# Performance work log

Hardware: AMD Instinct MI355X
Metric: run time of the kernel (lower is better)

The kernel has to match this reference:

```python
import jax, jax.numpy as jnp
import numpy as np

B, T, L, D = 2, 16, 256, 1152
NH, HD = 16, 72
MLP_H = int(int(D * 4.0) * 2 / 3)  # 3072, per SwiGLUFFN


def _rms(x, w, eps=1e-6):
    return x * jax.lax.rsqrt(jnp.mean(jnp.square(x), axis=-1, keepdims=True) + eps) * w


def _attn(x, qkv_w, qkv_b, qn, kn, proj_w, proj_b, nh):
    Bn, N, C = x.shape
    hd = C // nh
    qkv = (x @ qkv_w + qkv_b).reshape(Bn, N, 3, nh, hd)
    qkv = jnp.transpose(qkv, (2, 0, 3, 1, 4))  # [3, Bn, nh, N, hd]
    q, k, v = qkv[0], qkv[1], qkv[2]
    q = _rms(q, qn)
    k = _rms(k, kn)
    scores = jnp.einsum('bhnd,bhmd->bhnm', q, k) / jnp.sqrt(jnp.float32(hd))
    a = jax.nn.softmax(scores, axis=-1)
    o = jnp.einsum('bhnm,bhmd->bhnd', a, v)
    o = jnp.transpose(o, (0, 2, 1, 3)).reshape(Bn, N, C)
    return o @ proj_w + proj_b


def setup_inputs() -> dict:
    key = jax.random.key(0)
    ks = jax.random.split(key, 12)
    w = lambda k, shape: jax.random.normal(k, shape, jnp.float32) * 0.02
    return {
        'x': jax.random.normal(ks[0], (B, T, L, D), jnp.float32),
        'c': jax.random.normal(ks[1], (B, D), jnp.float32),
        'norm1_w': jnp.ones((D,), jnp.float32),
        'norm2_w': jnp.ones((D,), jnp.float32),
        'norm3_w': jnp.ones((D,), jnp.float32),
        'qn_s': jnp.ones((HD,), jnp.float32),
        'kn_s': jnp.ones((HD,), jnp.float32),
        'qkv_s_w': w(ks[2], (D, 3 * D)),
        'qkv_s_b': jnp.zeros((3 * D,), jnp.float32),
        'proj_s_w': w(ks[3], (D, D)),
        'proj_s_b': jnp.zeros((D,), jnp.float32),
        'qn_t': jnp.ones((HD,), jnp.float32),
        'kn_t': jnp.ones((HD,), jnp.float32),
        'qkv_t_w': w(ks[4], (D, 3 * D)),
        'qkv_t_b': jnp.zeros((3 * D,), jnp.float32),
        'proj_t_w': w(ks[5], (D, D)),
        'proj_t_b': jnp.zeros((D,), jnp.float32),
        'w12_w': w(ks[6], (D, 2 * MLP_H)),
        'w12_b': jnp.zeros((2 * MLP_H,), jnp.float32),
        'w3_w': w(ks[7], (MLP_H, D)),
        'w3_b': jnp.zeros((D,), jnp.float32),
        'ada_w': w(ks[8], (D, 9 * D)),
        'ada_b': jnp.zeros((9 * D,), jnp.float32),
    }


def reference(x, c, norm1_w, norm2_w, norm3_w,
              qn_s, kn_s, qkv_s_w, qkv_s_b, proj_s_w, proj_s_b,
              qn_t, kn_t, qkv_t_w, qkv_t_b, proj_t_w, proj_t_b,
              w12_w, w12_b, w3_w, w3_b, ada_w, ada_b):
    Bb, Tt, Ll, Dd = x.shape
    # adaLN_modulation: SiLU then Linear, chunk into 9 [B, D] tensors
    ch = (jax.nn.silu(c) @ ada_w + ada_b).reshape(Bb, 9, Dd)
    sh_s, sc_s, g_s = ch[:, 0], ch[:, 1], ch[:, 2]
    sh_t, sc_t, g_t = ch[:, 3], ch[:, 4], ch[:, 5]
    sh_m, sc_m, g_m = ch[:, 6], ch[:, 7], ch[:, 8]

    # spatial attention over L, folded batch B*T
    x_s = x.reshape(Bb * Tt, Ll, Dd)
    shs = jnp.repeat(sh_s, Tt, axis=0)[:, None, :]   # [B*T,1,D]
    scs = jnp.repeat(sc_s, Tt, axis=0)[:, None, :]
    gs = jnp.repeat(g_s, Tt, axis=0)[:, None, :]
    xn = _rms(x_s, norm1_w) * (1 + scs) + shs
    x_s = x_s + gs * _attn(xn, qkv_s_w, qkv_s_b, qn_s, kn_s, proj_s_w, proj_s_b, NH)
    x = x_s.reshape(Bb, Tt, Ll, Dd)

    # temporal attention over T, folded batch B*L
    x_t = jnp.transpose(x, (0, 2, 1, 3)).reshape(Bb * Ll, Tt, Dd)
    sht = jnp.repeat(sh_t, Ll, axis=0)[:, None, :]
    sct = jnp.repeat(sc_t, Ll, axis=0)[:, None, :]
    gt = jnp.repeat(g_t, Ll, axis=0)[:, None, :]
    xn = _rms(x_t, norm2_w) * (1 + sct) + sht
    x_t = x_t + gt * _attn(xn, qkv_t_w, qkv_t_b, qn_t, kn_t, proj_t_w, proj_t_b, NH)
    x = jnp.transpose(x_t.reshape(Bb, Ll, Tt, Dd), (0, 2, 1, 3))

    # SwiGLU MLP with adaLN modulate + gate
    xn = _rms(x, norm3_w) * (1 + sc_m[:, None, None, :]) + sh_m[:, None, None, :]
    x12 = xn @ w12_w + w12_b
    x1, x2 = jnp.split(x12, 2, axis=-1)
    mlp_out = (jax.nn.silu(x1) * x2) @ w3_w + w3_b
    x = x + g_m[:, None, None, :] * mlp_out
    return x
```

## Files before the change

kernel.cpp:

```cpp
#include <hip/hip_runtime.h>
#include <stdint.h>

typedef __bf16 bf16x8 __attribute__((ext_vector_type(8)));
typedef float f32x4 __attribute__((ext_vector_type(4)));

__device__ __forceinline__ float b2f(uint32_t u) {
  union { uint32_t i; float f; } v; v.i = u << 16; return v.f;
}
__device__ __forceinline__ uint16_t f2b(float f) {
  union { float f; uint32_t i; } v; v.f = f;
  uint32_t r = (v.i + 0x7fffu + ((v.i >> 16) & 1u)) >> 16;
  return (uint16_t)r;
}
__device__ __forceinline__ void unpack8(uint4 u, float* f) {
  f[0] = b2f(u.x & 0xffffu); f[1] = b2f(u.x >> 16);
  f[2] = b2f(u.y & 0xffffu); f[3] = b2f(u.y >> 16);
  f[4] = b2f(u.z & 0xffffu); f[5] = b2f(u.z >> 16);
  f[6] = b2f(u.w & 0xffffu); f[7] = b2f(u.w >> 16);
}

__device__ __forceinline__ void gl2lds16(const void* g, void* l) {
  __builtin_amdgcn_global_load_lds(
      (const __attribute__((address_space(1))) void*)g,
      (__attribute__((address_space(3))) void*)l, 16, 0, 0);
}

__global__ __launch_bounds__(512, 2) void gemm256_k(
    const uint16_t* __restrict__ A, int lda,
    const uint16_t* __restrict__ Bt,
    const float* __restrict__ bias,
    uint16_t* __restrict__ outb,
    float* __restrict__ outf, const float* __restrict__ resid,
    const float* __restrict__ gate,
    int N, int K, int mode)
{
  __shared__ __align__(16) uint16_t L[65536];
  const int tid = threadIdx.x;
  const int lane = tid & 63, wave = tid >> 6;
  const int l15 = lane & 15, quad = lane >> 4;
  const int wm = (wave >> 2) * 128, wn = (wave & 3) * 64;

  const int xcd = blockIdx.x & 7;
  const int slot = blockIdx.x >> 3;
  const int mt = xcd * 4 + (slot & 3);
  const int nt = slot >> 2;
  const int row0 = mt * 256, col0 = nt * 256;

  const int NTk = K >> 6;

  const uint16_t* Ag = A + (size_t)row0 * lda;
  const uint16_t* Bg = Bt + (size_t)col0 * K;

  const int sX = (lane & 7) ^ (lane >> 3);
  const int laneRowA = lane >> 3;
  const int laneK8A = sX * 8;
  const int laneRowB = 2 * (lane >> 3) + ((sX >> 2) & 1);
  const int laneK8B = (sX & 3) * 8;
  const int rA0 = ((wave * 16) & 63) + (((wave * 16) >> 6) << 7);
  const int rB0 = wave * 32;

#define STAGE_A(BUF, SUB, KT) do { \
    const uint16_t* g_ = Ag + (size_t)(rA0 + (SUB) * 64 + laneRowA) * lda + (size_t)(KT) * 64 + laneK8A; \
    uint16_t* l_ = (uint16_t*)&L[(BUF) * 32768 + (rA0 + (SUB) * 64) * 64]; \
    gl2lds16(g_, l_); \
    gl2lds16(g_ + (size_t)8 * lda, l_ + 512); \
  } while (0)

#define STAGE_B(BUF, HALF, KT) do { \
    const uint16_t* g_ = Bg + (size_t)(rB0 + laneRowB) * K + (size_t)(KT) * 64 + (HALF) * 32 + laneK8B; \
    uint16_t* l_ = (uint16_t*)&L[(BUF) * 32768 + 16384 + (HALF) * 8192 + rB0 * 32]; \
    gl2lds16(g_, l_); \
    gl2lds16(g_ + (size_t)16 * K, l_ + 512); \
  } while (0)

  f32x4 acc[8][4];
#pragma unroll
  for (int i = 0; i < 8; i++)
#pragma unroll
    for (int j = 0; j < 4; j++)
      acc[i][j] = (f32x4){0.f, 0.f, 0.f, 0.f};

  bf16x8 a_[4], b_[4];

#define PHASE(CUR, KK, QM, READB, STAGE_STMT, VM_STMT) do { \
    _Pragma("unroll") for (int mi = 0; mi < 4; mi++) \
      a_[mi] = *(const bf16x8*)&L[(CUR) * 32768 + (wm + (QM) * 64 + mi * 16 + l15) * 64 + \
                                  ((((KK) * 4 + quad) ^ (l15 & 7)) * 8)]; \
    if (READB) { \
      _Pragma("unroll") for (int ni = 0; ni < 4; ni++) \
        b_[ni] = *(const bf16x8*)&L[(CUR) * 32768 + 16384 + (KK) * 8192 + \
                                    ((wn >> 1) + ni * 8 + (l15 >> 1)) * 64 + \
                                    ((((((l15 & 1) << 2) | quad)) ^ (l15 >> 1)) * 8)]; \
    } \
    STAGE_STMT; \
    __builtin_amdgcn_sched_barrier(0); \
    __builtin_amdgcn_s_barrier(); \
    asm volatile("s_waitcnt lgkmcnt(0)" ::: "memory"); \
    __builtin_amdgcn_sched_barrier(0); \
    __builtin_amdgcn_s_setprio(1); \
    _Pragma("unroll") for (int mi = 0; mi < 4; mi++) \
      _Pragma("unroll") for (int ni = 0; ni < 4; ni++) \
        acc[(QM) * 4 + mi][ni] = __builtin_amdgcn_mfma_f32_16x16x32_bf16( \
            a_[mi], b_[ni], acc[(QM) * 4 + mi][ni], 0, 0, 0); \
    __builtin_amdgcn_s_setprio(0); \
    __builtin_amdgcn_sched_barrier(0); \
    VM_STMT; \
    __builtin_amdgcn_sched_barrier(0); \
    __builtin_amdgcn_s_barrier(); \
    __builtin_amdgcn_sched_barrier(0); \
  } while (0)

#define TILE(CUR, T) do { \
    PHASE(CUR, 0, 0, 1, { if ((T) + 1 < NTk) STAGE_B((CUR) ^ 1, 1, (T) + 1); }, {}); \
    PHASE(CUR, 0, 1, 0, { if ((T) + 1 < NTk) STAGE_A((CUR) ^ 1, 1, (T) + 1); }, {}); \
    PHASE(CUR, 1, 0, 1, { if ((T) + 2 < NTk) STAGE_B((CUR), 0, (T) + 2); }, {}); \
    PHASE(CUR, 1, 1, 0, { if ((T) + 2 < NTk) STAGE_A((CUR), 0, (T) + 2); }, \
      { if ((T) + 2 < NTk) { asm volatile("s_waitcnt vmcnt(4)" ::: "memory"); } \
        else               { asm volatile("s_waitcnt vmcnt(0)" ::: "memory"); } }); \
  } while (0)

  STAGE_A(0, 0, 0); STAGE_A(0, 1, 0); STAGE_B(0, 0, 0); STAGE_B(0, 1, 0);
  STAGE_A(1, 0, 1); STAGE_B(1, 0, 1);
  asm volatile("s_waitcnt vmcnt(4)" ::: "memory");
  __builtin_amdgcn_sched_barrier(0);
  __builtin_amdgcn_s_barrier();
  __builtin_amdgcn_sched_barrier(0);

  for (int t = 0; t < NTk; t += 2) {
    TILE(0, t);
    TILE(1, t + 1);
  }

#undef PHASE
#undef TILE
#undef STAGE_A
#undef STAGE_B

#pragma unroll
  for (int mi = 0; mi < 8; mi++) {
#pragma unroll
    for (int ni = 0; ni < 4; ni++) {
      const int colg = col0 + wn + ni * 16 + l15;
      if (colg < N) {
        const float bv = bias ? bias[colg] : 0.f;
#pragma unroll
        for (int i = 0; i < 4; i++) {
          const int rowg = row0 + wm + mi * 16 + quad * 4 + i;
          const float v = acc[mi][ni][i] + bv;
          const size_t idx = (size_t)rowg * N + colg;
          if (mode == 0) {
            outb[idx] = f2b(v);
          } else {
            const int b = rowg >> 12;
            outf[idx] = resid[idx] + gate[b * 10368 + colg] * v;
          }
        }
      }
    }
  }
}

__global__ __launch_bounds__(256) void rmsnorm_k(
    const float* __restrict__ x, const float* __restrict__ w,
    const float* __restrict__ chv, int shsel, int scsel,
    uint16_t* __restrict__ xn)
{
  const int row = blockIdx.x;
  const int b = row >> 12;
  const float* xr = x + (size_t)row * 1152;
  float ss = 0.f;
  for (int d = threadIdx.x; d < 1152; d += 256) { const float v = xr[d]; ss += v * v; }
  for (int off = 32; off > 0; off >>= 1) ss += __shfl_down(ss, off);
  __shared__ float red[4];
  if ((threadIdx.x & 63) == 0) red[threadIdx.x >> 6] = ss;
  __syncthreads();
  const float tot = red[0] + red[1] + red[2] + red[3];
  const float rs = rsqrtf(tot * (1.f / 1152.f) + 1e-6f);
  const float* sh = chv + b * 10368 + shsel * 1152;
  const float* sc = chv + b * 10368 + scsel * 1152;
  uint16_t* xo = xn + (size_t)row * 1152;
  for (int d = threadIdx.x; d < 1152; d += 256)
    xo[d] = f2b(xr[d] * rs * w[d] * (1.f + sc[d]) + sh[d]);
}

__global__ __launch_bounds__(256) void qknorm_k(
    uint16_t* __restrict__ qkv, const float* __restrict__ qn, const float* __restrict__ kn)
{
  const int tid = threadIdx.x;
  const int rl = tid >> 5, unit = tid & 31;
  const int h = unit & 15, isK = unit >> 4;
  const size_t row = (size_t)blockIdx.x * 8 + rl;
  uint16_t* p = qkv + row * 3456 + isK * 1152 + h * 72;
  const float* w = isK ? kn : qn;
  float v[72];
#pragma unroll
  for (int i = 0; i < 9; i++) unpack8(((const uint4*)p)[i], v + i * 8);
  float ss = 0.f;
#pragma unroll
  for (int d = 0; d < 72; d++) ss += v[d] * v[d];
  const float rs = rsqrtf(ss * (1.f / 72.f) + 1e-6f);
#pragma unroll
  for (int d = 0; d < 72; d++) p[d] = f2b(v[d] * rs * w[d]);
}

#define AK_STRIDE 104
#define VT_STRIDE 88
#define PS_STRIDE 72
__global__ __launch_bounds__(256) void attn_s_k(
    const uint16_t* __restrict__ qkv, uint16_t* __restrict__ out)
{
  __shared__ __align__(16) uint16_t Ks[64 * AK_STRIDE];
  __shared__ __align__(16) uint16_t Vt[80 * VT_STRIDE];
  __shared__ __align__(16) uint16_t Ps[4 * 64 * PS_STRIDE];
  const int bh = blockIdx.x;
  const int bt = bh >> 4, h = bh & 15;
  const int tid = threadIdx.x;
  const int lane = tid & 63, wave = tid >> 6;
  const int l15 = lane & 15, quad = lane >> 4;
  const size_t rowbase = (size_t)bt * 256;
  const float scale = 0.1178511301977579f;

  union { uint4 u; bf16x8 v; } zu; zu.u = make_uint4(0, 0, 0, 0);
  const bf16x8 zero8 = zu.v;

  bf16x8 qf[4][3];
#pragma unroll
  for (int mi = 0; mi < 4; mi++) {
    const uint16_t* qp = qkv + (rowbase + wave * 64 + mi * 16 + l15) * 3456 + h * 72;
    qf[mi][0] = *(const bf16x8*)(qp + quad * 8);
    qf[mi][1] = *(const bf16x8*)(qp + 32 + quad * 8);
    qf[mi][2] = (quad == 0) ? *(const bf16x8*)(qp + 64) : zero8;
  }

  f32x4 oacc[4][5];
#pragma unroll
  for (int mi = 0; mi < 4; mi++)
#pragma unroll
    for (int dt = 0; dt < 5; dt++)
      oacc[mi][dt] = (f32x4){0.f, 0.f, 0.f, 0.f};
  float mrun[4][4], lrun[4][4];
#pragma unroll
  for (int mi = 0; mi < 4; mi++)
#pragma unroll
    for (int i = 0; i < 4; i++) { mrun[mi][i] = -1e30f; lrun[mi][i] = 0.f; }

  uint16_t* psw = &Ps[wave * 64 * PS_STRIDE];

  for (int c = 0; c < 4; c++) {
    __syncthreads();
    for (int idx = tid; idx < 576; idx += 256) {
      const int rr = idx / 9, cc = idx - rr * 9;
      const uint16_t* kg = qkv + (rowbase + c * 64 + rr) * 3456 + 1152 + h * 72 + cc * 8;
      *(uint4*)&Ks[rr * AK_STRIDE + cc * 8] = *(const uint4*)kg;
      uint4 vv = *(const uint4*)(kg + 1152);
      const uint16_t* e = (const uint16_t*)&vv;
#pragma unroll
      for (int j = 0; j < 8; j++) Vt[(cc * 8 + j) * VT_STRIDE + rr] = e[j];
    }
    __syncthreads();

    f32x4 s[4][4];
#pragma unroll
    for (int mi = 0; mi < 4; mi++)
#pragma unroll
      for (int ni = 0; ni < 4; ni++)
        s[mi][ni] = (f32x4){0.f, 0.f, 0.f, 0.f};
#pragma unroll
    for (int ni = 0; ni < 4; ni++) {
      bf16x8 kf0 = *(const bf16x8*)&Ks[(ni * 16 + l15) * AK_STRIDE + quad * 8];
      bf16x8 kf1 = *(const bf16x8*)&Ks[(ni * 16 + l15) * AK_STRIDE + 32 + quad * 8];
      bf16x8 kf2 = (quad == 0) ? *(const bf16x8*)&Ks[(ni * 16 + l15) * AK_STRIDE + 64] : zero8;
#pragma unroll
      for (int mi = 0; mi < 4; mi++) {
        s[mi][ni] = __builtin_amdgcn_mfma_f32_16x16x32_bf16(qf[mi][0], kf0, s[mi][ni], 0, 0, 0);
        s[mi][ni] = __builtin_amdgcn_mfma_f32_16x16x32_bf16(qf[mi][1], kf1, s[mi][ni], 0, 0, 0);
        s[mi][ni] = __builtin_amdgcn_mfma_f32_16x16x32_bf16(qf[mi][2], kf2, s[mi][ni], 0, 0, 0);
      }
    }

#pragma unroll
    for (int mi = 0; mi < 4; mi++) {
#pragma unroll
      for (int i = 0; i < 4; i++) {
        float mx = fmaxf(fmaxf(s[mi][0][i], s[mi][1][i]), fmaxf(s[mi][2][i], s[mi][3][i])) * scale;
#pragma unroll
        for (int d = 1; d < 16; d <<= 1) mx = fmaxf(mx, __shfl_xor(mx, d));
        const float mnew = fmaxf(mrun[mi][i], mx);
        const float corr = __expf(mrun[mi][i] - mnew);
        mrun[mi][i] = mnew;
        float psum = 0.f;
#pragma unroll
        for (int ni = 0; ni < 4; ni++) {
          const float p = __expf(s[mi][ni][i] * scale - mnew);
          s[mi][ni][i] = p;
          psum += p;
        }
#pragma unroll
        for (int d = 1; d < 16; d <<= 1) psum += __shfl_xor(psum, d);
        lrun[mi][i] = lrun[mi][i] * corr + psum;
#pragma unroll
        for (int dt = 0; dt < 5; dt++) oacc[mi][dt][i] *= corr;
      }
    }

#pragma unroll
    for (int mi = 0; mi < 4; mi++)
#pragma unroll
      for (int ni = 0; ni < 4; ni++)
#pragma unroll
        for (int i = 0; i < 4; i++)
          psw[(mi * 16 + quad * 4 + i) * PS_STRIDE + ni * 16 + l15] = f2b(s[mi][ni][i]);

#pragma unroll
    for (int kk = 0; kk < 2; kk++) {
      bf16x8 pf[4];
#pragma unroll
      for (int mi = 0; mi < 4; mi++)
        pf[mi] = *(const bf16x8*)&psw[(mi * 16 + l15) * PS_STRIDE + kk * 32 + quad * 8];
#pragma unroll
      for (int dt = 0; dt < 5; dt++) {
        bf16x8 vf = *(const bf16x8*)&Vt[(dt * 16 + l15) * VT_STRIDE + kk * 32 + quad * 8];
#pragma unroll
        for (int mi = 0; mi < 4; mi++)
          oacc[mi][dt] = __builtin_amdgcn_mfma_f32_16x16x32_bf16(pf[mi], vf, oacc[mi][dt], 0, 0, 0);
      }
    }
  }

#pragma unroll
  for (int mi = 0; mi < 4; mi++) {
#pragma unroll
    for (int i = 0; i < 4; i++) {
      const float inv = 1.f / lrun[mi][i];
      const size_t orow = rowbase + wave * 64 + mi * 16 + quad * 4 + i;
#pragma unroll
      for (int dt = 0; dt < 5; dt++) {
        const int d = dt * 16 + l15;
        if (d < 72) out[orow * 1152 + h * 72 + d] = f2b(oacc[mi][dt][i] * inv);
      }
    }
  }
}

__global__ __launch_bounds__(128) void attn_t_k(
    const uint16_t* __restrict__ qkv, uint16_t* __restrict__ out)
{
  const int blk = blockIdx.x;
  const int bl = blk >> 1, hg = blk & 1;
  const int b = bl >> 8, l = bl & 255;
  const int tid = threadIdx.x;
  const int hh = tid >> 4, tq = tid & 15;
  const int h = hg * 8 + hh;
  __shared__ __align__(16) uint16_t kb[8 * 16 * 72];
  __shared__ __align__(16) uint16_t vb[8 * 16 * 72];

#pragma unroll
  for (int it = 0; it < 9; it++) {
    const int idx = tid + it * 128;
    const int rowL = idx / 9, cc = idx % 9;
    const int hhL = rowL >> 4, tL = rowL & 15;
    const size_t grow = (size_t)b * 4096 + (size_t)tL * 256 + l;
    const int colk = 1152 + (hg * 8 + hhL) * 72 + cc * 8;
    ((uint4*)&kb[rowL * 72])[cc] = *(const uint4*)(qkv + grow * 3456 + colk);
    ((uint4*)&vb[rowL * 72])[cc] = *(const uint4*)(qkv + grow * 3456 + colk + 1152);
  }
  __syncthreads();

  float q[72];
  const size_t qrow = (size_t)b * 4096 + (size_t)tq * 256 + l;
  {
    const uint16_t* qp = qkv + qrow * 3456 + h * 72;
#pragma unroll
    for (int i = 0; i < 9; i++) unpack8(((const uint4*)qp)[i], q + i * 8);
  }
  const float scale = 0.1178511301977579f;
  float s[16];
#pragma unroll
  for (int m = 0; m < 16; m++) {
    const uint4* kr = (const uint4*)&kb[(hh * 16 + m) * 72];
    float a = 0.f;
#pragma unroll
    for (int i = 0; i < 9; i++) {
      float kf[8]; unpack8(kr[i], kf);
#pragma unroll
      for (int j = 0; j < 8; j++) a += q[i * 8 + j] * kf[j];
    }
    s[m] = a * scale;
  }
  float mx = -1e30f;
#pragma unroll
  for (int m = 0; m < 16; m++) mx = fmaxf(mx, s[m]);
  float sum = 0.f;
#pragma unroll
  for (int m = 0; m < 16; m++) { s[m] = __expf(s[m] - mx); sum += s[m]; }
  const float inv = 1.f / sum;
  float o[72];
#pragma unroll
  for (int d = 0; d < 72; d++) o[d] = 0.f;
#pragma unroll
  for (int m = 0; m < 16; m++) {
    const float p = s[m];
    const uint4* vr = (const uint4*)&vb[(hh * 16 + m) * 72];
#pragma unroll
    for (int i = 0; i < 9; i++) {
      float vf[8]; unpack8(vr[i], vf);
#pragma unroll
      for (int j = 0; j < 8; j++) o[i * 8 + j] += p * vf[j];
    }
  }
  uint16_t* op = out + qrow * 1152 + h * 72;
#pragma unroll
  for (int d = 0; d < 72; d++) op[d] = f2b(o[d] * inv);
}

__global__ __launch_bounds__(256) void transcvt_k(
    const float* __restrict__ in, uint16_t* __restrict__ out, int K, int N)
{
  __shared__ float t[32][33];
  const int n0 = blockIdx.x * 32, k0 = blockIdx.y * 32;
  const int tx = threadIdx.x & 31, ty = threadIdx.x >> 5;
#pragma unroll
  for (int i = 0; i < 32; i += 8)
    t[ty + i][tx] = in[(size_t)(k0 + ty + i) * N + n0 + tx];
  __syncthreads();
#pragma unroll
  for (int i = 0; i < 32; i += 8)
    out[(size_t)(n0 + ty + i) * K + k0 + tx] = f2b(t[tx][ty + i]);
}

__global__ __launch_bounds__(256) void swiglu_k(uint16_t* __restrict__ x12)
{
  const size_t gid = (size_t)blockIdx.x * 256 + threadIdx.x;
  const size_t row = gid / 384, c8 = gid - row * 384;
  uint4* base = (uint4*)(x12 + row * 6144);
  float a[8], bb[8];
  unpack8(base[c8], a);
  unpack8(base[384 + c8], bb);
  uint32_t r[4];
#pragma unroll
  for (int j = 0; j < 4; j++) {
    const float s0 = a[2 * j]     / (1.f + __expf(-a[2 * j]))     * bb[2 * j];
    const float s1 = a[2 * j + 1] / (1.f + __expf(-a[2 * j + 1])) * bb[2 * j + 1];
    r[j] = (uint32_t)f2b(s0) | ((uint32_t)f2b(s1) << 16);
  }
  base[c8] = make_uint4(r[0], r[1], r[2], r[3]);
}

__global__ void siluc_k(const float* __restrict__ c, float* __restrict__ cs) {
  const int i = blockIdx.x * 256 + threadIdx.x;
  if (i < 2304) { const float v = c[i]; cs[i] = v / (1.f + __expf(-v)); }
}

#define ADA_KS 18
#define ADA_RK 64
__global__ __launch_bounds__(256) void ada_part_k(
    const float* __restrict__ cs, const float* __restrict__ W,
    float* __restrict__ part)
{
  const int col = blockIdx.x * 256 + threadIdx.x;
  const int ks = blockIdx.y;
  const int k0 = ks * ADA_RK;
  __shared__ float sc0[ADA_RK], sc1[ADA_RK];
  if (threadIdx.x < ADA_RK) sc0[threadIdx.x] = cs[k0 + threadIdx.x];
  else if (threadIdx.x < 2 * ADA_RK) sc1[threadIdx.x - ADA_RK] = cs[1152 + k0 + threadIdx.x - ADA_RK];
  __syncthreads();
  if (col >= 10368) return;
  const float* Wp = W + (size_t)k0 * 10368 + col;
  float s0 = 0.f, s1 = 0.f;
#pragma unroll 8
  for (int r = 0; r < ADA_RK; r++) {
    const float wv = Wp[(size_t)r * 10368];
    s0 += sc0[r] * wv;
    s1 += sc1[r] * wv;
  }
  part[(size_t)(ks * 2 + 0) * 10368 + col] = s0;
  part[(size_t)(ks * 2 + 1) * 10368 + col] = s1;
}

__global__ __launch_bounds__(256) void ada_reduce_k(
    const float* __restrict__ part, const float* __restrict__ bias,
    float* __restrict__ chv)
{
  const int col = blockIdx.x * 256 + threadIdx.x;
  if (col >= 10368) return;
  float s0 = bias[col], s1 = bias[col];
#pragma unroll
  for (int ks = 0; ks < ADA_KS; ks++) {
    s0 += part[(size_t)(ks * 2 + 0) * 10368 + col];
    s1 += part[(size_t)(ks * 2 + 1) * 10368 + col];
  }
  chv[col] = s0;
  chv[10368 + col] = s1;
}

extern "C" void kernel_launch(void* const* d_in, const int* in_sizes, int n_in,
                              void* d_out, int out_size, void* d_ws, size_t ws_size,
                              hipStream_t stream)
{
  const float* c_in    = (const float*)d_in[1];
  const float* norm1w  = (const float*)d_in[2];
  const float* norm2w  = (const float*)d_in[3];
  const float* norm3w  = (const float*)d_in[4];
  const float* qn_s    = (const float*)d_in[5];
  const float* kn_s    = (const float*)d_in[6];
  const float* qkv_s_w = (const float*)d_in[7];
  const float* qkv_s_b = (const float*)d_in[8];
  const float* proj_s_w= (const float*)d_in[9];
  const float* proj_s_b= (const float*)d_in[10];
  const float* qn_t    = (const float*)d_in[11];
  const float* kn_t    = (const float*)d_in[12];
  const float* qkv_t_w = (const float*)d_in[13];
  const float* qkv_t_b = (const float*)d_in[14];
  const float* proj_t_w= (const float*)d_in[15];
  const float* proj_t_b= (const float*)d_in[16];
  const float* w12_w   = (const float*)d_in[17];
  const float* w12_b   = (const float*)d_in[18];
  const float* w3_w    = (const float*)d_in[19];
  const float* w3_b    = (const float*)d_in[20];
  const float* ada_w   = (const float*)d_in[21];
  const float* ada_b   = (const float*)d_in[22];

  float* X = (float*)d_out;

  char* wsb = (char*)d_ws; size_t off = 0;
  auto alloc = [&](size_t bytes) -> void* {
    void* p = wsb + off; off += bytes; off = (off + 255) & ~(size_t)255; return p;
  };
  uint16_t* XN    = (uint16_t*)alloc((size_t)8192 * 1152 * 2);
  uint16_t* QKV   = (uint16_t*)alloc((size_t)8192 * 6144 * 2);
  uint16_t* X12   = QKV;
  uint16_t* WqkvS = (uint16_t*)alloc((size_t)3584 * 1152 * 2);
  uint16_t* WprojS= (uint16_t*)alloc((size_t)1280 * 1152 * 2);
  uint16_t* WqkvT = (uint16_t*)alloc((size_t)3584 * 1152 * 2);
  uint16_t* WprojT= (uint16_t*)alloc((size_t)1280 * 1152 * 2);
  uint16_t* W12T  = (uint16_t*)alloc((size_t)6144 * 1152 * 2);
  uint16_t* W3T   = (uint16_t*)alloc((size_t)1280 * 3072 * 2);
  float* CH = (float*)alloc((size_t)2 * 10368 * 4);
  float* CS = (float*)alloc((size_t)2 * 1152 * 4);
  float* APART = (float*)alloc((size_t)ADA_KS * 2 * 10368 * 4);

  hipMemcpyAsync(X, d_in[0], (size_t)8192 * 1152 * 4, hipMemcpyDeviceToDevice, stream);
  siluc_k<<<9, 256, 0, stream>>>(c_in, CS);
  ada_part_k<<<dim3(41, ADA_KS), 256, 0, stream>>>(CS, ada_w, APART);
  ada_reduce_k<<<41, 256, 0, stream>>>(APART, ada_b, CH);

  transcvt_k<<<dim3(3456 / 32, 1152 / 32), 256, 0, stream>>>(qkv_s_w, WqkvS, 1152, 3456);
  transcvt_k<<<dim3(1152 / 32, 1152 / 32), 256, 0, stream>>>(proj_s_w, WprojS, 1152, 1152);
  transcvt_k<<<dim3(3456 / 32, 1152 / 32), 256, 0, stream>>>(qkv_t_w, WqkvT, 1152, 3456);
  transcvt_k<<<dim3(1152 / 32, 1152 / 32), 256, 0, stream>>>(proj_t_w, WprojT, 1152, 1152);
  transcvt_k<<<dim3(6144 / 32, 1152 / 32), 256, 0, stream>>>(w12_w, W12T, 1152, 6144);
  transcvt_k<<<dim3(1152 / 32, 3072 / 32), 256, 0, stream>>>(w3_w, W3T, 3072, 1152);

  rmsnorm_k<<<8192, 256, 0, stream>>>(X, norm1w, CH, 0, 1, XN);
  gemm256_k<<<32 * 14, 512, 0, stream>>>(XN, 1152, WqkvS, qkv_s_b, QKV, nullptr, nullptr, nullptr,
                                         3456, 1152, 0);
  qknorm_k<<<1024, 256, 0, stream>>>(QKV, qn_s, kn_s);
  attn_s_k<<<512, 256, 0, stream>>>(QKV, XN);
  gemm256_k<<<32 * 5, 512, 0, stream>>>(XN, 1152, WprojS, proj_s_b, nullptr, X, X, CH + 2 * 1152,
                                        1152, 1152, 1);

  rmsnorm_k<<<8192, 256, 0, stream>>>(X, norm2w, CH, 3, 4, XN);
  gemm256_k<<<32 * 14, 512, 0, stream>>>(XN, 1152, WqkvT, qkv_t_b, QKV, nullptr, nullptr, nullptr,
                                         3456, 1152, 0);
  qknorm_k<<<1024, 256, 0, stream>>>(QKV, qn_t, kn_t);
  attn_t_k<<<1024, 128, 0, stream>>>(QKV, XN);
  gemm256_k<<<32 * 5, 512, 0, stream>>>(XN, 1152, WprojT, proj_t_b, nullptr, X, X, CH + 5 * 1152,
                                        1152, 1152, 1);

  rmsnorm_k<<<8192, 256, 0, stream>>>(X, norm3w, CH, 6, 7, XN);
  gemm256_k<<<32 * 24, 512, 0, stream>>>(XN, 1152, W12T, w12_b, X12, nullptr, nullptr, nullptr,
                                         6144, 1152, 0);
  swiglu_k<<<12288, 256, 0, stream>>>(X12);
  gemm256_k<<<32 * 5, 512, 0, stream>>>(X12, 6144, W3T, w3_b, nullptr, X, X, CH + 8 * 1152,
                                        1152, 3072, 1);
}
```

Measured before the change: 1.078 ms.

## Double-buffer LDS fragment registers to overlap reads with MFMA in GEMM mainloop

Restructures the GEMM inner loop so that the A/B fragments for the next phase are read from LDS into a second register set while the current phase's MFMAs run. It drops the per-phase lgkmcnt(0) wait and one barrier per phase, and changes the vmcnt accounting so the next tile's data is ready before its first fragments are prefetched. This hides LDS read latency behind matrix math, at the cost of more VGPRs (two fragment sets) and more delicate barrier and waitcnt ordering that could race if miscounted.

```diff
diff --git a/kernel.cpp b/kernel.cpp
--- a/kernel.cpp
+++ b/kernel.cpp
@@ -80,61 +80,78 @@
     for (int j = 0; j < 4; j++)
       acc[i][j] = (f32x4){0.f, 0.f, 0.f, 0.f};
 
-  bf16x8 a_[4], b_[4];
-
-#define PHASE(CUR, KK, QM, READB, STAGE_STMT, VM_STMT) do { \
+  bf16x8 aA[4], aB[4], bA[4], bB[4];
+
+#define READ_A(BUF, DST, QM, KK) do { \
     _Pragma("unroll") for (int mi = 0; mi < 4; mi++) \
-      a_[mi] = *(const bf16x8*)&L[(CUR) * 32768 + (wm + (QM) * 64 + mi * 16 + l15) * 64 + \
-                                  ((((KK) * 4 + quad) ^ (l15 & 7)) * 8)]; \
-    if (READB) { \
-      _Pragma("unroll") for (int ni = 0; ni < 4; ni++) \
-        b_[ni] = *(const bf16x8*)&L[(CUR) * 32768 + 16384 + (KK) * 8192 + \
-                                    ((wn >> 1) + ni * 8 + (l15 >> 1)) * 64 + \
-                                    ((((((l15 & 1) << 2) | quad)) ^ (l15 >> 1)) * 8)]; \
-    } \
-    STAGE_STMT; \
-    __builtin_amdgcn_sched_barrier(0); \
-    __builtin_amdgcn_s_barrier(); \
-    asm volatile("s_waitcnt lgkmcnt(0)" ::: "memory"); \
-    __builtin_amdgcn_sched_barrier(0); \
+      DST[mi] = *(const bf16x8*)&L[(BUF) * 32768 + (wm + (QM) * 64 + mi * 16 + l15) * 64 + \
+                                   ((((KK) * 4 + quad) ^ (l15 & 7)) * 8)]; \
+  } while (0)
+
+#define READ_B(BUF, DST, KK) do { \
+    _Pragma("unroll") for (int ni = 0; ni < 4; ni++) \
+      DST[ni] = *(const bf16x8*)&L[(BUF) * 32768 + 16384 + (KK) * 8192 + \
+                                   ((wn >> 1) + ni * 8 + (l15 >> 1)) * 64 + \
+                                   ((((((l15 & 1) << 2) | quad)) ^ (l15 >> 1)) * 8)]; \
+  } while (0)
+
+#define MFMA16(QM, AF, BF) do { \
     __builtin_amdgcn_s_setprio(1); \
     _Pragma("unroll") for (int mi = 0; mi < 4; mi++) \
       _Pragma("unroll") for (int ni = 0; ni < 4; ni++) \
         acc[(QM) * 4 + mi][ni] = __builtin_amdgcn_mfma_f32_16x16x32_bf16( \
-            a_[mi], b_[ni], acc[(QM) * 4 + mi][ni], 0, 0, 0); \
+            AF[mi], BF[ni], acc[(QM) * 4 + mi][ni], 0, 0, 0); \
     __builtin_amdgcn_s_setprio(0); \
-    __builtin_amdgcn_sched_barrier(0); \
-    VM_STMT; \
-    __builtin_amdgcn_sched_barrier(0); \
-    __builtin_amdgcn_s_barrier(); \
-    __builtin_amdgcn_sched_barrier(0); \
   } while (0)
 
+#define SB __builtin_amdgcn_sched_barrier(0)
+#define BAR __builtin_amdgcn_s_barrier()
+
 #define TILE(CUR, T) do { \
-    PHASE(CUR, 0, 0, 1, { if ((T) + 1 < NTk) STAGE_B((CUR) ^ 1, 1, (T) + 1); }, {}); \
-    PHASE(CUR, 0, 1, 0, { if ((T) + 1 < NTk) STAGE_A((CUR) ^ 1, 1, (T) + 1); }, {}); \
-    PHASE(CUR, 1, 0, 1, { if ((T) + 2 < NTk) STAGE_B((CUR), 0, (T) + 2); }, {}); \
-    PHASE(CUR, 1, 1, 0, { if ((T) + 2 < NTk) STAGE_A((CUR), 0, (T) + 2); }, \
-      { if ((T) + 2 < NTk) { asm volatile("s_waitcnt vmcnt(4)" ::: "memory"); } \
-        else               { asm volatile("s_waitcnt vmcnt(0)" ::: "memory"); } }); \
+     \
+    READ_A(CUR, aB, 1, 0); SB; \
+    MFMA16(0, aA, bA); \
+    if ((T) + 1 < NTk) STAGE_B((CUR) ^ 1, 1, (T) + 1); \
+    SB; BAR; SB; \
+     \
+    READ_A(CUR, aA, 0, 1); READ_B(CUR, bB, 1); SB; \
+    MFMA16(1, aB, bA); \
+    if ((T) + 1 < NTk) STAGE_A((CUR) ^ 1, 1, (T) + 1); \
+    SB; BAR; SB; \
+     \
+    READ_A(CUR, aB, 1, 1); SB; \
+    MFMA16(0, aA, bB); \
+    if ((T) + 2 < NTk) STAGE_B((CUR), 0, (T) + 2); \
+    SB; BAR; SB; \
+     \
+    if ((T) + 2 < NTk) { asm volatile("s_waitcnt vmcnt(2)" ::: "memory"); } \
+    else               { asm volatile("s_waitcnt vmcnt(0)" ::: "memory"); } \
+    SB; BAR; SB; \
+    READ_A((CUR) ^ 1, aA, 0, 0); READ_B((CUR) ^ 1, bA, 0); SB; \
+    MFMA16(1, aB, bB); \
+    if ((T) + 2 < NTk) STAGE_A((CUR), 0, (T) + 2); \
+    SB; BAR; SB; \
   } while (0)
 
   STAGE_A(0, 0, 0); STAGE_A(0, 1, 0); STAGE_B(0, 0, 0); STAGE_B(0, 1, 0);
   STAGE_A(1, 0, 1); STAGE_B(1, 0, 1);
   asm volatile("s_waitcnt vmcnt(4)" ::: "memory");
-  __builtin_amdgcn_sched_barrier(0);
-  __builtin_amdgcn_s_barrier();
-  __builtin_amdgcn_sched_barrier(0);
+  SB; BAR; SB;
+  READ_A(0, aA, 0, 0); READ_B(0, bA, 0); SB;
 
   for (int t = 0; t < NTk; t += 2) {
     TILE(0, t);
     TILE(1, t + 1);
   }
 
-#undef PHASE
 #undef TILE
+#undef READ_A
+#undef READ_B
+#undef MFMA16
 #undef STAGE_A
 #undef STAGE_B
+#undef SB
+#undef BAR
 
 #pragma unroll
   for (int mi = 0; mi < 8; mi++) {
```

After: 1.430 ms. +32.6%, slower.

## Add 128x128 GEMM kernel for non-256-aligned shapes, drop padded weight buffers

Applied to the files above, without the earlier changes.

Adds a simpler 128x128-tile, 256-thread GEMM with double-buffered direct-to-LDS loads and a swizzled layout. It is used for the QKV, projection and W3 GEMMs, whose N dimensions (3456, 1152) do not divide by 256. This removes the wasted compute on padded columns and gives better wave quantization on the small-N projection GEMMs, which previously launched only 160 blocks. The large 256-tile kernel is kept only for the W12 GEMM, with its bounds check and residual mode removed. The trade-off is that the smaller tiles reuse less data per block and the simple pipeline has less latency hiding than the tuned 256 kernel.

```diff
diff --git a/kernel.cpp b/kernel.cpp
--- a/kernel.cpp
+++ b/kernel.cpp
@@ -25,7 +25,7 @@
       (__attribute__((address_space(3))) void*)l, 16, 0, 0);
 }
 
-__global__ __launch_bounds__(512, 2) void gemm256_k(
+__global__ __launch_bounds__(256) void gemm_k(
     const uint16_t* __restrict__ A, int lda,
     const uint16_t* __restrict__ Bt,
     const float* __restrict__ bias,
@@ -33,6 +33,93 @@
     float* __restrict__ outf, const float* __restrict__ resid,
     const float* __restrict__ gate,
     int N, int K, int mode)
+{
+  __shared__ __align__(16) uint16_t As[2][128 * 32];
+  __shared__ __align__(16) uint16_t Bs[2][128 * 32];
+  const int tid = threadIdx.x;
+  const int xcd = blockIdx.x & 7;
+  const int slot = blockIdx.x >> 3;
+  const int mt = xcd * 8 + (slot & 7);
+  const int nt = slot >> 3;
+  const int row0 = mt * 128, col0 = nt * 128;
+
+  const int lane = tid & 63, wave = tid >> 6;
+  const int l15 = lane & 15, quad = lane >> 4;
+  const int wm = (wave & 1) * 64, wn = (wave >> 1) * 64;
+
+  f32x4 acc[4][4];
+  const f32x4 zero = {0.f, 0.f, 0.f, 0.f};
+  for (int i = 0; i < 4; i++)
+    for (int j = 0; j < 4; j++)
+      acc[i][j] = zero;
+
+  const int rseg = wave * 32 + (lane >> 2);
+  const int kseg8 = (((lane & 3) ^ ((lane >> 2) & 3) ^ ((lane >> 4) & 3))) * 8;
+  const uint16_t* gA = A + (size_t)(row0 + rseg) * lda + kseg8;
+  const uint16_t* gB = Bt + (size_t)(col0 + rseg) * K + kseg8;
+  const size_t rowA16 = (size_t)16 * lda;
+  const size_t rowB16 = (size_t)16 * K;
+  const int woff = wave * 2048;
+
+  const int gsw = ((quad ^ (l15 & 3) ^ ((l15 >> 2) & 3))) * 8;
+
+  gl2lds16(gA,          (char*)As[0] + woff);
+  gl2lds16(gA + rowA16, (char*)As[0] + woff + 1024);
+  gl2lds16(gB,          (char*)Bs[0] + woff);
+  gl2lds16(gB + rowB16, (char*)Bs[0] + woff + 1024);
+
+  for (int k0 = 0; k0 < K; k0 += 32) {
+    const int cur = (k0 >> 5) & 1;
+    __syncthreads();
+    if (k0 + 32 < K) {
+      const int nxt = cur ^ 1;
+      gl2lds16(gA + k0 + 32,          (char*)As[nxt] + woff);
+      gl2lds16(gA + rowA16 + k0 + 32, (char*)As[nxt] + woff + 1024);
+      gl2lds16(gB + k0 + 32,          (char*)Bs[nxt] + woff);
+      gl2lds16(gB + rowB16 + k0 + 32, (char*)Bs[nxt] + woff + 1024);
+    }
+
+    bf16x8 af[4], bfr[4];
+#pragma unroll
+    for (int i = 0; i < 4; i++) {
+      af[i]  = *(const bf16x8*)&As[cur][(wm + i * 16 + l15) * 32 + gsw];
+      bfr[i] = *(const bf16x8*)&Bs[cur][(wn + i * 16 + l15) * 32 + gsw];
+    }
+#pragma unroll
+    for (int mi = 0; mi < 4; mi++)
+#pragma unroll
+      for (int ni = 0; ni < 4; ni++)
+        acc[mi][ni] = __builtin_amdgcn_mfma_f32_16x16x32_bf16(af[mi], bfr[ni], acc[mi][ni], 0, 0, 0);
+  }
+
+#pragma unroll
+  for (int mi = 0; mi < 4; mi++) {
+#pragma unroll
+    for (int ni = 0; ni < 4; ni++) {
+      const int colg = col0 + wn + ni * 16 + l15;
+      const float bv = bias ? bias[colg] : 0.f;
+#pragma unroll
+      for (int i = 0; i < 4; i++) {
+        const int rowg = row0 + wm + mi * 16 + quad * 4 + i;
+        const float v = acc[mi][ni][i] + bv;
+        const size_t idx = (size_t)rowg * N + colg;
+        if (mode == 0) {
+          outb[idx] = f2b(v);
+        } else {
+          const int b = rowg >> 12;
+          outf[idx] = resid[idx] + gate[b * 10368 + colg] * v;
+        }
+      }
+    }
+  }
+}
+
+__global__ __launch_bounds__(512, 2) void gemm256_k(
+    const uint16_t* __restrict__ A, int lda,
+    const uint16_t* __restrict__ Bt,
+    const float* __restrict__ bias,
+    uint16_t* __restrict__ outb,
+    int N, int K)
 {
   __shared__ __align__(16) uint16_t L[65536];
   const int tid = threadIdx.x;
@@ -141,20 +228,11 @@
 #pragma unroll
     for (int ni = 0; ni < 4; ni++) {
       const int colg = col0 + wn + ni * 16 + l15;
-      if (colg < N) {
-        const float bv = bias ? bias[colg] : 0.f;
-#pragma unroll
-        for (int i = 0; i < 4; i++) {
-          const int rowg = row0 + wm + mi * 16 + quad * 4 + i;
-          const float v = acc[mi][ni][i] + bv;
-          const size_t idx = (size_t)rowg * N + colg;
-          if (mode == 0) {
-            outb[idx] = f2b(v);
-          } else {
-            const int b = rowg >> 12;
-            outf[idx] = resid[idx] + gate[b * 10368 + colg] * v;
-          }
-        }
+      const float bv = bias[colg];
+#pragma unroll
+      for (int i = 0; i < 4; i++) {
+        const int rowg = row0 + wm + mi * 16 + quad * 4 + i;
+        outb[(size_t)rowg * N + colg] = f2b(acc[mi][ni][i] + bv);
       }
     }
   }
@@ -529,12 +607,12 @@
   uint16_t* XN    = (uint16_t*)alloc((size_t)8192 * 1152 * 2);
   uint16_t* QKV   = (uint16_t*)alloc((size_t)8192 * 6144 * 2);
   uint16_t* X12   = QKV;
-  uint16_t* WqkvS = (uint16_t*)alloc((size_t)3584 * 1152 * 2);
-  uint16_t* WprojS= (uint16_t*)alloc((size_t)1280 * 1152 * 2);
-  uint16_t* WqkvT = (uint16_t*)alloc((size_t)3584 * 1152 * 2);
-  uint16_t* WprojT= (uint16_t*)alloc((size_t)1280 * 1152 * 2);
+  uint16_t* WqkvS = (uint16_t*)alloc((size_t)3456 * 1152 * 2);
+  uint16_t* WprojS= (uint16_t*)alloc((size_t)1152 * 1152 * 2);
+  uint16_t* WqkvT = (uint16_t*)alloc((size_t)3456 * 1152 * 2);
+  uint16_t* WprojT= (uint16_t*)alloc((size_t)1152 * 1152 * 2);
   uint16_t* W12T  = (uint16_t*)alloc((size_t)6144 * 1152 * 2);
-  uint16_t* W3T   = (uint16_t*)alloc((size_t)1280 * 3072 * 2);
+  uint16_t* W3T   = (uint16_t*)alloc((size_t)1152 * 3072 * 2);
   float* CH = (float*)alloc((size_t)2 * 10368 * 4);
   float* CS = (float*)alloc((size_t)2 * 1152 * 4);
   float* APART = (float*)alloc((size_t)ADA_KS * 2 * 10368 * 4);
@@ -552,25 +630,24 @@
   transcvt_k<<<dim3(1152 / 32, 3072 / 32), 256, 0, stream>>>(w3_w, W3T, 3072, 1152);
 
   rmsnorm_k<<<8192, 256, 0, stream>>>(X, norm1w, CH, 0, 1, XN);
-  gemm256_k<<<32 * 14, 512, 0, stream>>>(XN, 1152, WqkvS, qkv_s_b, QKV, nullptr, nullptr, nullptr,
-                                         3456, 1152, 0);
+  gemm_k<<<27 * 64, 256, 0, stream>>>(XN, 1152, WqkvS, qkv_s_b, QKV, nullptr, nullptr, nullptr,
+                                      3456, 1152, 0);
   qknorm_k<<<1024, 256, 0, stream>>>(QKV, qn_s, kn_s);
   attn_s_k<<<512, 256, 0, stream>>>(QKV, XN);
-  gemm256_k<<<32 * 5, 512, 0, stream>>>(XN, 1152, WprojS, proj_s_b, nullptr, X, X, CH + 2 * 1152,
-                                        1152, 1152, 1);
+  gemm_k<<<9 * 64, 256, 0, stream>>>(XN, 1152, WprojS, proj_s_b, nullptr, X, X, CH + 2 * 1152,
+                                     1152, 1152, 1);
 
   rmsnorm_k<<<8192, 256, 0, stream>>>(X, norm2w, CH, 3, 4, XN);
-  gemm256_k<<<32 * 14, 512, 0, stream>>>(XN, 1152, WqkvT, qkv_t_b, QKV, nullptr, nullptr, nullptr,
-                                         3456, 1152, 0);
+  gemm_k<<<27 * 64, 256, 0, stream>>>(XN, 1152, WqkvT, qkv_t_b, QKV, nullptr, nullptr, nullptr,
+                                      3456, 1152, 0);
   qknorm_k<<<1024, 256, 0, stream>>>(QKV, qn_t, kn_t);
   attn_t_k<<<1024, 128, 0, stream>>>(QKV, XN);
-  gemm256_k<<<32 * 5, 512, 0, stream>>>(XN, 1152, WprojT, proj_t_b, nullptr, X, X, CH + 5 * 1152,
-                                        1152, 1152, 1);
+  gemm_k<<<9 * 64, 256, 0, stream>>>(XN, 1152, WprojT, proj_t_b, nullptr, X, X, CH + 5 * 1152,
+                                     1152, 1152, 1);
 
   rmsnorm_k<<<8192, 256, 0, stream>>>(X, norm3w, CH, 6, 7, XN);
-  gemm256_k<<<32 * 24, 512, 0, stream>>>(XN, 1152, W12T, w12_b, X12, nullptr, nullptr, nullptr,
-                                         6144, 1152, 0);
+  gemm256_k<<<32 * 24, 512, 0, stream>>>(XN, 1152, W12T, w12_b, X12, 6144, 1152);
   swiglu_k<<<12288, 256, 0, stream>>>(X12);
-  gemm256_k<<<32 * 5, 512, 0, stream>>>(X12, 6144, W3T, w3_b, nullptr, X, X, CH + 8 * 1152,
-                                        1152, 3072, 1);
-}
+  gemm_k<<<9 * 64, 256, 0, stream>>>(X12, 6144, W3T, w3_b, nullptr, X, X, CH + 8 * 1152,
+                                     1152, 3072, 1);
+}
```

New measurement: 993.8 us. 7.8% less time.
